# Kernel tuning notes

Hardware: AMD Instinct MI355X
Metric: run time of the kernel (lower is better)

Reference implementation:

```python
import jax, jax.numpy as jnp
import numpy as np

N_HEADS = 16
N_KV_HEADS = 4
HEAD_DIM = 128


def apply_rotary_emb(x, cos, sin):
    # x: [B, S, H, D]; cos/sin: [S, D//2]
    xr = x[..., 0::2]
    xi = x[..., 1::2]
    c = cos[None, :, None, :]
    s = sin[None, :, None, :]
    out_r = xr * c - xi * s
    out_i = xr * s + xi * c
    # interleave back: [..., D//2, 2] -> [..., D]
    return jnp.stack([out_r, out_i], axis=-1).reshape(x.shape)


def setup_inputs() -> dict:
    key = jax.random.key(0)
    ks = jax.random.split(key, 7)
    B, S, D = 4, 2048, 2048
    x = jax.random.normal(ks[0], (B, S, D), dtype=jnp.float32)
    # realistic rotary tables
    inv_freq = 1.0 / (10000.0 ** (jnp.arange(0, HEAD_DIM, 2, dtype=jnp.float32) / HEAD_DIM))
    t = jnp.arange(S, dtype=jnp.float32)
    freqs = jnp.outer(t, inv_freq)  # [S, D/2]
    freqs_cos = jnp.cos(freqs)
    freqs_sin = jnp.sin(freqs)
    sc = 0.02
    wq = jax.random.normal(ks[1], (D, N_HEADS * HEAD_DIM), dtype=jnp.float32) * sc
    wk = jax.random.normal(ks[2], (D, N_KV_HEADS * HEAD_DIM), dtype=jnp.float32) * sc
    wv = jax.random.normal(ks[3], (D, N_KV_HEADS * HEAD_DIM), dtype=jnp.float32) * sc
    wo = jax.random.normal(ks[4], (N_HEADS * HEAD_DIM, D), dtype=jnp.float32) * sc
    return {"x": x, "freqs_cos": freqs_cos, "freqs_sin": freqs_sin,
            "wq": wq, "wk": wk, "wv": wv, "wo": wo}


def reference(x, freqs_cos, freqs_sin, wq, wk, wv, wo):
    B, S, D = x.shape
    n_rep = N_HEADS // N_KV_HEADS
    xq = (x @ wq).reshape(B, S, N_HEADS, HEAD_DIM)
    xk = (x @ wk).reshape(B, S, N_KV_HEADS, HEAD_DIM)
    xv = (x @ wv).reshape(B, S, N_KV_HEADS, HEAD_DIM)
    xq = apply_rotary_emb(xq, freqs_cos, freqs_sin)
    xk = apply_rotary_emb(xk, freqs_cos, freqs_sin)
    # repeat_kv (GQA): [B,S,Hkv,D] -> [B,S,Hkv*n_rep,D]
    xk = jnp.repeat(xk, n_rep, axis=2)
    xv = jnp.repeat(xv, n_rep, axis=2)
    # [B,H,S,D]
    q = xq.transpose(0, 2, 1, 3)
    k = xk.transpose(0, 2, 1, 3)
    v = xv.transpose(0, 2, 1, 3)
    scores = jnp.einsum('bhqd,bhkd->bhqk', q, k) / jnp.sqrt(jnp.float32(HEAD_DIM))
    causal = jnp.triu(jnp.ones((S, S), dtype=bool), k=1)
    scores = jnp.where(causal[None, None], -jnp.inf, scores)
    probs = jax.nn.softmax(scores, axis=-1)
    out = jnp.einsum('bhqk,bhkd->bhqd', probs, v)
    out = out.transpose(0, 2, 1, 3).reshape(B, S, N_HEADS * HEAD_DIM)
    return out @ wo
```

## Files before the change

### kernel.cpp

```cpp
#include <hip/hip_runtime.h>
#include <stdint.h>
#include <stddef.h>

#define B_ 4
#define S_ 2048
#define D_ 2048
#define NH 16
#define NKV 4
#define HD 128
#define QKV_N 3072
#define ROWS (B_*S_)

typedef unsigned short u16;
typedef __attribute__((ext_vector_type(8))) unsigned short u16x8;
typedef __attribute__((ext_vector_type(8))) __bf16 bf16x8;
typedef __attribute__((ext_vector_type(4))) float f32x4;

__device__ __forceinline__ u16 f2bf(float f) {
  unsigned u = __builtin_bit_cast(unsigned, f);
  return (u16)((u + 0x7fffu + ((u >> 16) & 1u)) >> 16);
}
__device__ __forceinline__ float bf2f(u16 h) {
  return __builtin_bit_cast(float, (unsigned)h << 16);
}
__device__ __forceinline__ f32x4 mfma16(u16x8 a, u16x8 b, f32x4 c) {
  return __builtin_amdgcn_mfma_f32_16x16x32_bf16(
      __builtin_bit_cast(bf16x8, a), __builtin_bit_cast(bf16x8, b), c, 0, 0, 0);
}
__device__ __forceinline__ void gld16(const void* g, void* l) {
  __builtin_amdgcn_global_load_lds(
      (const __attribute__((address_space(1))) void*)g,
      (__attribute__((address_space(3))) void*)l, 16, 0, 0);
}

__global__ __launch_bounds__(256) void k_cast_x(const float* __restrict__ x, u16* __restrict__ xb) {
  int i = blockIdx.x * 256 + threadIdx.x;
  float4 v = ((const float4*)x)[i];
  union { u16 u[4]; uint2 p; } o;
  o.u[0] = f2bf(v.x); o.u[1] = f2bf(v.y); o.u[2] = f2bf(v.z); o.u[3] = f2bf(v.w);
  ((uint2*)xb)[i] = o.p;
}

__global__ __launch_bounds__(256) void k_wt(const float* __restrict__ w, u16* __restrict__ wt, int K, int N) {
  __shared__ float tile[32][33];
  int kb = blockIdx.y * 32, nb = blockIdx.x * 32;
  int tx = threadIdx.x, ty = threadIdx.y;
#pragma unroll
  for (int j = 0; j < 32; j += 8)
    tile[ty + j][tx] = w[(size_t)(kb + ty + j) * N + nb + tx];
  __syncthreads();
#pragma unroll
  for (int j = 0; j < 32; j += 8)
    wt[(size_t)(nb + ty + j) * K + kb + tx] = f2bf(tile[tx][ty + j]);
}


#define STG_A(KK, SS) do {                                                   \
    gld16(Ag + (size_t)r0 * 2048 + (KK) + coff, As + (SS) * 8192 + stl0);    \
    gld16(Ag + (size_t)(r0 + 128) * 2048 + (KK) + coff,                      \
          As + (SS) * 8192 + stl1);                                          \
  } while (0)
#define STG_B(KK, SS) do {                                                   \
    gld16(Bg + (size_t)r0 * 2048 + (KK) + coff, Bs + (SS) * 8192 + stl0);    \
    gld16(Bg + (size_t)(r0 + 128) * 2048 + (KK) + coff,                      \
          Bs + (SS) * 8192 + stl1);                                          \
  } while (0)

#define PHASE(RS, MB, RB, SS, SK, SA, VM) do {                               \
    const u16* Ap_ = As + (RS) * 8192;                                       \
    _Pragma("unroll") for (int i_ = 0; i_ < 4; ++i_)                         \
      af[i_] = *(const u16x8*)(Ap_ + arow0 + ((MB) + i_) * 512);             \
    if (RB) {                                                                \
      const u16* Bp_ = Bs + (RS) * 8192;                                     \
      _Pragma("unroll") for (int i_ = 0; i_ < 4; ++i_)                       \
        bf[i_] = *(const u16x8*)(Bp_ + brow0 + i_ * 512);                    \
    }                                                                        \
    if (SA) STG_A(SK, SS); else STG_B(SK, SS);                               \
    asm volatile("s_barrier" ::: "memory");                                  \
    asm volatile("s_waitcnt lgkmcnt(0)" ::: "memory");                       \
    __builtin_amdgcn_sched_barrier(0);                                       \
    __builtin_amdgcn_s_setprio(1);                                           \
    _Pragma("unroll") for (int i_ = 0; i_ < 4; ++i_)                         \
      _Pragma("unroll") for (int n_ = 0; n_ < 4; ++n_)                       \
        acc[(MB) + i_][n_] = mfma16(af[i_], bf[n_], acc[(MB) + i_][n_]);     \
    __builtin_amdgcn_s_setprio(0);                                           \
    __builtin_amdgcn_sched_barrier(0);                                       \
    if (VM) asm volatile("s_waitcnt vmcnt(8)" ::: "memory");                 \
    asm volatile("s_barrier" ::: "memory");                                  \
  } while (0)

template<int NT, bool F32OUT>
__global__ __launch_bounds__(512, 2) void k_gemm(const u16* __restrict__ A, const u16* __restrict__ Bt,
                                                 void* __restrict__ C) {
  __shared__ u16 As[4 * 8192];
  __shared__ u16 Bs[4 * 8192];
  int id = blockIdx.x;
  int nwg = gridDim.x;
  id = (id & 7) * (nwg >> 3) + (id >> 3);
  const int gx = NT / 256;
  int mb = (id / gx) * 256, nb = (id % gx) * 256;

  int t = threadIdx.x;
  int l = t & 63, L16 = l & 15, quad = l >> 4;
  int w = t >> 6, wm = w >> 2, wn = w & 3;
  const int schunk = 8 * (quad ^ ((L16 >> 1) & 3));
  const int arow0 = (wm * 128 + L16) * 32 + schunk;
  const int brow0 = (wn * 64 + L16) * 32 + schunk;
  const int r0 = t >> 2;
  const int coff = 8 * ((t & 3) ^ ((r0 >> 1) & 3));
  const int stl0 = (t & 448) * 8, stl1 = stl0 + 4096;

  const u16* Ag = A + (size_t)mb * 2048;
  const u16* Bg = Bt + (size_t)nb * 2048;
  u16x8 af[4], bf[4];
  f32x4 acc[8][4] = {};

  STG_A(0, 0);  STG_B(0, 0);
  STG_A(32, 1); STG_B(32, 1);
  STG_A(64, 2); STG_B(64, 2);
  asm volatile("s_waitcnt vmcnt(8)" ::: "memory");
  asm volatile("s_barrier" ::: "memory");

#pragma unroll 2
  for (int tt = 0; tt < 32; ++tt) {
    int rs0 = (2 * tt) & 3, rs1 = (2 * tt + 1) & 3;
    int ss1 = (2 * tt + 3) & 3;
    int k1n = ((tt + 1) & 31) * 64 + 32;
    int k0n = ((tt + 2) & 31) * 64;
    PHASE(rs0, 0, true,  ss1, k1n, true,  false);
    PHASE(rs0, 4, false, ss1, k1n, false, true);
    PHASE(rs1, 0, true,  rs0, k0n, true,  false);
    PHASE(rs1, 4, false, rs0, k0n, false, true);
  }
  asm volatile("s_waitcnt vmcnt(0)" ::: "memory");

#pragma unroll
  for (int m = 0; m < 8; ++m)
#pragma unroll
    for (int n = 0; n < 4; ++n)
#pragma unroll
      for (int r = 0; r < 4; ++r) {
        int row = mb + wm * 128 + m * 16 + quad * 4 + r;
        int col = nb + wn * 64 + n * 16 + L16;
        if constexpr (F32OUT)
          ((float*)C)[(size_t)row * NT + col] = acc[m][n][r];
        else
          ((u16*)C)[(size_t)row * NT + col] = f2bf(acc[m][n][r]);
      }
}

__global__ __launch_bounds__(256) void k_rope(const u16* __restrict__ qkv, const float* __restrict__ fc,
                                              const float* __restrict__ fs, u16* __restrict__ Q,
                                              u16* __restrict__ Kk) {
  const float SC = 0.1275174214f;
  int row = blockIdx.x;
  int b = row >> 11, s = row & 2047;
  int t = threadIdx.x;
#pragma unroll
  for (int j = 0; j < 5; ++j) {
    int p = t + j * 256;
    int i = p & 63;
    float c = fc[s * 64 + i], sn = fs[s * 64 + i];
    if (p < 1024) {
      int h = p >> 6;
      unsigned pr = *(const unsigned*)(qkv + (size_t)row * QKV_N + h * 128 + 2 * i);
      float xr = bf2f((u16)(pr & 0xffff)), xi = bf2f((u16)(pr >> 16));
      size_t o = (((size_t)(b * NH + h) * S_) + s) * HD + 2 * i;
      unsigned out = (unsigned)f2bf((xr * c - xi * sn) * SC) |
                     ((unsigned)f2bf((xr * sn + xi * c) * SC) << 16);
      *(unsigned*)(Q + o) = out;
    } else {
      int kh = (p - 1024) >> 6;
      unsigned pr = *(const unsigned*)(qkv + (size_t)row * QKV_N + 2048 + kh * 128 + 2 * i);
      float xr = bf2f((u16)(pr & 0xffff)), xi = bf2f((u16)(pr >> 16));
      size_t o = (((size_t)(b * NKV + kh) * S_) + s) * HD + 2 * i;
      unsigned out = (unsigned)f2bf(xr * c - xi * sn) | ((unsigned)f2bf(xr * sn + xi * c) << 16);
      *(unsigned*)(Kk + o) = out;
    }
  }
}

__global__ __launch_bounds__(256) void k_vt(const u16* __restrict__ qkv, u16* __restrict__ Vt) {
  __shared__ u16 tile[64 * 128];
  int blk = blockIdx.x;
  int sb = blk & 31, kh = (blk >> 5) & 3, b = blk >> 7;
  int t = threadIdx.x;
  int s0 = sb * 64;
#pragma unroll
  for (int i = 0; i < 4; ++i) {
    int lin = i * 256 + t;
    int row = lin >> 4, c = lin & 15;
    u16x8 v = *(const u16x8*)(qkv + (size_t)(b * S_ + s0 + row) * QKV_N + 2560 + kh * HD + c * 8);
    *(u16x8*)(tile + row * 128 + ((c ^ (row & 15)) * 8)) = v;
  }
  __syncthreads();
#pragma unroll
  for (int i = 0; i < 2; ++i) {
    int u = i * 256 + t;
    int p = u >> 3, o = u & 7;
    u16 lo[8], hi[8];
#pragma unroll
    for (int j = 0; j < 8; ++j) {
      int s = o * 8 + j;
      int cs = (p >> 2) ^ (s & 15);
      unsigned v = *(const unsigned*)(tile + s * 128 + cs * 8 + (p & 3) * 2);
      lo[j] = (u16)(v & 0xffff); hi[j] = (u16)(v >> 16);
    }
    size_t ob = ((size_t)(b * NKV + kh) * HD + 2 * p) * S_ + s0 + o * 8;
    *(u16x8*)(Vt + ob)      = *(u16x8*)lo;
    *(u16x8*)(Vt + ob + S_) = *(u16x8*)hi;
  }
}

__global__ __launch_bounds__(256) void k_attn(const u16* __restrict__ Q, const u16* __restrict__ Kg,
                                              const u16* __restrict__ Vt, u16* __restrict__ O) {
  int bx = blockIdx.x;
  int bh = bx >> 3, pr = bx & 7;
  int b = bh >> 4, h = bh & 15, kh = h >> 2;
  int t = threadIdx.x;
  int w = t >> 6, l = t & 63, L = l & 15, quad = l >> 4;

  __shared__ u16 Ks[64 * 128];
  __shared__ u16 Vs[128 * 64];
  __shared__ u16 Ps[4][32 * 72];
  u16* Pw = &Ps[w][0];

  const u16* Qh = Q  + ((size_t)(b * NH  + h ) * S_) * HD;
  const u16* Kh = Kg + ((size_t)(b * NKV + kh) * S_) * HD;
  const u16* Vh = Vt + ((size_t)(b * NKV + kh) * HD) * S_;

  u16x8 ones;
#pragma unroll
  for (int i = 0; i < 8; ++i) ones[i] = 0x3F80;

  int koff[4], voff[2];
#pragma unroll
  for (int kk = 0; kk < 4; ++kk) koff[kk] = 128 * L + 8 * ((4 * kk + quad) ^ (L & 7));
#pragma unroll
  for (int kc = 0; kc < 2; ++kc) voff[kc] = 64 * L + 8 * ((4 * kc + quad) ^ (L & 7));
  const int pread  = 72 * L + 8 * quad;
  const int pwrite = 72 * L + 4 * quad;

  int kgo[4], vgo[4], klo[4], vlo[4];
#pragma unroll
  for (int i = 0; i < 4; ++i) {
    int lin = i * 256 + t;
    int row = lin >> 4, c = lin & 15;
    kgo[i] = row * HD + ((c ^ (row & 7)) * 8);
    int d = lin >> 3, c2 = lin & 7;
    vgo[i] = d * S_ + ((c2 ^ (d & 7)) * 8);
    klo[i] = (i * 256 + (t & 192)) * 8;
    vlo[i] = (i * 256 + (t & 192)) * 8;
  }

#pragma unroll 1
  for (int half = 0; half < 2; ++half) {
    int qb = half ? (15 - pr) : pr;
    int q0 = qb * 128 + w * 32;

    u16x8 qf[2][4];
#pragma unroll
    for (int m = 0; m < 2; ++m)
#pragma unroll
      for (int kk = 0; kk < 4; ++kk)
        qf[m][kk] = *(const u16x8*)(Qh + (size_t)(q0 + m * 16 + L) * HD + kk * 32 + quad * 8);

    f32x4 acc[2][9] = {};
    int ktiles = 2 * qb + 2;
#pragma unroll 1
    for (int kt = 0; kt < ktiles; ++kt) {
      int kbase = kt * 64;
      __syncthreads();
      const u16* Kt = Kh + (size_t)kbase * HD;
      const u16* Vg = Vh + kbase;
#pragma unroll
      for (int i = 0; i < 4; ++i) gld16(Kt + kgo[i], Ks + klo[i]);
#pragma unroll
      for (int i = 0; i < 4; ++i) gld16(Vg + vgo[i], Vs + vlo[i]);
      __syncthreads();
      if (kbase > q0 + 31) continue;

      bool needMask = (kbase + 63 > q0);
#pragma unroll
      for (int n = 0; n < 4; ++n) {
        f32x4 s0v = {}, s1v = {};
#pragma unroll
        for (int kk = 0; kk < 4; ++kk) {
          u16x8 kf = *(const u16x8*)(Ks + koff[kk] + 2048 * n);
          s0v = mfma16(kf, qf[0][kk], s0v);
          s1v = mfma16(kf, qf[1][kk], s1v);
        }
#pragma unroll
        for (int m = 0; m < 2; ++m) {
          f32x4 sv = m ? s1v : s0v;
          int qrow = q0 + m * 16 + L;
          unsigned eu[4];
#pragma unroll
          for (int r = 0; r < 4; ++r) {
            float e = exp2f(sv[r]);
            if (needMask) {
              int key = kbase + n * 16 + quad * 4 + r;
              e = (key <= qrow) ? e : 0.0f;
            }
            eu[r] = __builtin_bit_cast(unsigned, e);
          }
          uint2 pk;
          pk.x = __builtin_amdgcn_perm(eu[1], eu[0], 0x07060302u);
          pk.y = __builtin_amdgcn_perm(eu[3], eu[2], 0x07060302u);
          *(uint2*)(Pw + pwrite + 1152 * m + 16 * n) = pk;
        }
      }
#pragma unroll
      for (int kc = 0; kc < 2; ++kc) {
        u16x8 pf0 = *(const u16x8*)(Pw + pread + 32 * kc);
        u16x8 pf1 = *(const u16x8*)(Pw + pread + 1152 + 32 * kc);
#pragma unroll
        for (int nt = 0; nt < 8; ++nt) {
          u16x8 vf = *(const u16x8*)(Vs + voff[kc] + 1024 * nt);
          acc[0][nt] = mfma16(pf0, vf, acc[0][nt]);
          acc[1][nt] = mfma16(pf1, vf, acc[1][nt]);
        }
        acc[0][8] = mfma16(pf0, ones, acc[0][8]);
        acc[1][8] = mfma16(pf1, ones, acc[1][8]);
      }
    }
#pragma unroll
    for (int m = 0; m < 2; ++m)
#pragma unroll
      for (int r = 0; r < 4; ++r) {
        float inv = 1.0f / acc[m][8][r];
        int qrow = q0 + m * 16 + quad * 4 + r;
#pragma unroll
        for (int nt = 0; nt < 8; ++nt) {
          int col = h * HD + nt * 16 + L;
          O[(size_t)(b * S_ + qrow) * D_ + col] = f2bf(acc[m][nt][r] * inv);
        }
      }
  }
}

extern "C" void kernel_launch(void* const* d_in, const int* in_sizes, int n_in,
                              void* d_out, int out_size, void* d_ws, size_t ws_size,
                              hipStream_t stream) {
  const float* x  = (const float*)d_in[0];
  const float* fc = (const float*)d_in[1];
  const float* fs = (const float*)d_in[2];
  const float* wq = (const float*)d_in[3];
  const float* wk = (const float*)d_in[4];
  const float* wv = (const float*)d_in[5];
  const float* wo = (const float*)d_in[6];
  float* out = (float*)d_out;

  u16* p = (u16*)d_ws;
  u16* xb    = p; p += (size_t)ROWS * D_;
  u16* wqkvT = p; p += (size_t)QKV_N * D_;
  u16* woT   = p; p += (size_t)D_ * D_;
  u16* qkv   = p; p += (size_t)ROWS * QKV_N;
  u16* Qr    = p; p += (size_t)ROWS * (NH * HD);
  u16* Kr    = p; p += (size_t)ROWS * (NKV * HD);
  u16* Vtr   = p; p += (size_t)ROWS * (NKV * HD);
  u16* AO    = p; p += (size_t)ROWS * D_;

  k_cast_x<<<dim3(ROWS * D_ / 1024), dim3(256), 0, stream>>>(x, xb);
  k_wt<<<dim3(64, 64), dim3(32, 8), 0, stream>>>(wq, wqkvT, 2048, 2048);
  k_wt<<<dim3(16, 64), dim3(32, 8), 0, stream>>>(wk, wqkvT + (size_t)2048 * 2048, 2048, 512);
  k_wt<<<dim3(16, 64), dim3(32, 8), 0, stream>>>(wv, wqkvT + (size_t)2560 * 2048, 2048, 512);
  k_wt<<<dim3(64, 64), dim3(32, 8), 0, stream>>>(wo, woT, 2048, 2048);
  k_gemm<QKV_N, false><<<dim3((QKV_N / 256) * (ROWS / 256)), dim3(512), 0, stream>>>(xb, wqkvT, qkv);
  k_rope<<<dim3(ROWS), dim3(256), 0, stream>>>(qkv, fc, fs, Qr, Kr);
  k_vt<<<dim3(B_ * NKV * (S_ / 64)), dim3(256), 0, stream>>>(qkv, Vtr);
  k_attn<<<dim3(64 * 8), dim3(256), 0, stream>>>(Qr, Kr, Vtr, AO);
  k_gemm<D_, true><<<dim3((D_ / 256) * (ROWS / 256)), dim3(512), 0, stream>>>(AO, woT, out);
}
```

Measured before the change: 458.8 us.

## Double-buffer LDS fragment registers to overlap LDS reads with MFMA in GEMM

```diff
diff --git a/kernel.cpp b/kernel.cpp
--- a/kernel.cpp
+++ b/kernel.cpp
@@ -66,26 +66,25 @@
           Bs + (SS) * 8192 + stl1);                                          \
   } while (0)
 
-#define PHASE(RS, MB, RB, SS, SK, SA, VM) do {                               \
-    const u16* Ap_ = As + (RS) * 8192;                                       \
+#define PH(AFU, BFU, MB, AFW, BFW, RDS, RDM, RDBF, SA, SK, SS, VM) do {      \
+    const u16* Rp_ = As + (RDS) * 8192;                                      \
     _Pragma("unroll") for (int i_ = 0; i_ < 4; ++i_)                         \
-      af[i_] = *(const u16x8*)(Ap_ + arow0 + ((MB) + i_) * 512);             \
-    if (RB) {                                                                \
-      const u16* Bp_ = Bs + (RS) * 8192;                                     \
+      AFW[i_] = *(const u16x8*)(Rp_ + arow0 + ((RDM) + i_) * 512);           \
+    if (RDBF) {                                                              \
+      const u16* Bp_ = Bs + (RDS) * 8192;                                    \
       _Pragma("unroll") for (int i_ = 0; i_ < 4; ++i_)                       \
-        bf[i_] = *(const u16x8*)(Bp_ + brow0 + i_ * 512);                    \
+        BFW[i_] = *(const u16x8*)(Bp_ + brow0 + i_ * 512);                   \
     }                                                                        \
     if (SA) STG_A(SK, SS); else STG_B(SK, SS);                               \
-    asm volatile("s_barrier" ::: "memory");                                  \
-    asm volatile("s_waitcnt lgkmcnt(0)" ::: "memory");                       \
     __builtin_amdgcn_sched_barrier(0);                                       \
     __builtin_amdgcn_s_setprio(1);                                           \
     _Pragma("unroll") for (int i_ = 0; i_ < 4; ++i_)                         \
       _Pragma("unroll") for (int n_ = 0; n_ < 4; ++n_)                       \
-        acc[(MB) + i_][n_] = mfma16(af[i_], bf[n_], acc[(MB) + i_][n_]);     \
+        acc[(MB) + i_][n_] = mfma16(AFU[i_], BFU[n_], acc[(MB) + i_][n_]);   \
     __builtin_amdgcn_s_setprio(0);                                           \
     __builtin_amdgcn_sched_barrier(0);                                       \
-    if (VM) asm volatile("s_waitcnt vmcnt(8)" ::: "memory");                 \
+    asm volatile("s_waitcnt lgkmcnt(0)" ::: "memory");                       \
+    if (VM) asm volatile("s_waitcnt vmcnt(6)" ::: "memory");                 \
     asm volatile("s_barrier" ::: "memory");                                  \
   } while (0)
 
@@ -112,7 +111,7 @@
 
   const u16* Ag = A + (size_t)mb * 2048;
   const u16* Bg = Bt + (size_t)nb * 2048;
-  u16x8 af[4], bf[4];
+  u16x8 afX[4], afY[4], bfX[4], bfY[4];
   f32x4 acc[8][4] = {};
 
   STG_A(0, 0);  STG_B(0, 0);
@@ -120,17 +119,25 @@
   STG_A(64, 2); STG_B(64, 2);
   asm volatile("s_waitcnt vmcnt(8)" ::: "memory");
   asm volatile("s_barrier" ::: "memory");
-
-#pragma unroll 2
-  for (int tt = 0; tt < 32; ++tt) {
-    int rs0 = (2 * tt) & 3, rs1 = (2 * tt + 1) & 3;
-    int ss1 = (2 * tt + 3) & 3;
-    int k1n = ((tt + 1) & 31) * 64 + 32;
-    int k0n = ((tt + 2) & 31) * 64;
-    PHASE(rs0, 0, true,  ss1, k1n, true,  false);
-    PHASE(rs0, 4, false, ss1, k1n, false, true);
-    PHASE(rs1, 0, true,  rs0, k0n, true,  false);
-    PHASE(rs1, 4, false, rs0, k0n, false, true);
+#pragma unroll
+  for (int i = 0; i < 4; ++i) {
+    afX[i] = *(const u16x8*)(As + arow0 + i * 512);
+    bfX[i] = *(const u16x8*)(Bs + brow0 + i * 512);
+  }
+
+#pragma unroll 1
+  for (int uu = 0; uu < 16; ++uu) {
+    int tA = 2 * uu, tB = 2 * uu + 1;
+    int a1 = ((tA + 1) & 31) * 64 + 32, a2 = ((tA + 2) & 31) * 64;
+    int b1 = ((tB + 1) & 31) * 64 + 32, b2 = ((tB + 2) & 31) * 64;
+    PH(afX, bfX, 0, afY, bfX, 0, 4, false, true,  a1, 3, true);
+    PH(afY, bfX, 4, afX, bfY, 1, 0, true,  false, a1, 3, false);
+    PH(afX, bfY, 0, afY, bfX, 1, 4, false, true,  a2, 0, true);
+    PH(afY, bfY, 4, afX, bfX, 2, 0, true,  false, a2, 0, false);
+    PH(afX, bfX, 0, afY, bfX, 2, 4, false, true,  b1, 1, true);
+    PH(afY, bfX, 4, afX, bfY, 3, 0, true,  false, b1, 1, false);
+    PH(afX, bfY, 0, afY, bfX, 3, 4, false, true,  b2, 2, true);
+    PH(afY, bfY, 4, afX, bfX, 0, 0, true,  false, b2, 2, false);
   }
   asm volatile("s_waitcnt vmcnt(0)" ::: "memory");
 
```

Measured after the change: 467.6 us. Within noise of the previous version (+1.9%).

## Restructure GEMM to 4 waves with 128x128 per-wave tiles

Applied to the files above, without the earlier changes.

```diff
diff --git a/kernel.cpp b/kernel.cpp
--- a/kernel.cpp
+++ b/kernel.cpp
@@ -55,42 +55,31 @@
 }
 
 
-#define STG_A(KK, SS) do {                                                   \
-    gld16(Ag + (size_t)r0 * 2048 + (KK) + coff, As + (SS) * 8192 + stl0);    \
-    gld16(Ag + (size_t)(r0 + 128) * 2048 + (KK) + coff,                      \
-          As + (SS) * 8192 + stl1);                                          \
+#define STG(GP, KK, SS, LB) do {                                             \
+    _Pragma("unroll") for (int j_ = 0; j_ < 4; ++j_)                         \
+      gld16(GP + (size_t)(j_ * 64 + r0) * 2048 + (KK) + coff,                \
+            LB + (SS) * 8192 + j_ * 2048 + stl);                             \
   } while (0)
-#define STG_B(KK, SS) do {                                                   \
-    gld16(Bg + (size_t)r0 * 2048 + (KK) + coff, Bs + (SS) * 8192 + stl0);    \
-    gld16(Bg + (size_t)(r0 + 128) * 2048 + (KK) + coff,                      \
-          Bs + (SS) * 8192 + stl1);                                          \
-  } while (0)
-
-#define PHASE(RS, MB, RB, SS, SK, SA, VM) do {                               \
+
+#define PH(RS, SS, KN) do {                                                  \
+    STG(Ag, KN, SS, As);                                                     \
+    STG(Bg, KN, SS, Bs);                                                     \
     const u16* Ap_ = As + (RS) * 8192;                                       \
-    _Pragma("unroll") for (int i_ = 0; i_ < 4; ++i_)                         \
-      af[i_] = *(const u16x8*)(Ap_ + arow0 + ((MB) + i_) * 512);             \
-    if (RB) {                                                                \
-      const u16* Bp_ = Bs + (RS) * 8192;                                     \
-      _Pragma("unroll") for (int i_ = 0; i_ < 4; ++i_)                       \
-        bf[i_] = *(const u16x8*)(Bp_ + brow0 + i_ * 512);                    \
-    }                                                                        \
-    if (SA) STG_A(SK, SS); else STG_B(SK, SS);                               \
-    asm volatile("s_barrier" ::: "memory");                                  \
-    asm volatile("s_waitcnt lgkmcnt(0)" ::: "memory");                       \
-    __builtin_amdgcn_sched_barrier(0);                                       \
-    __builtin_amdgcn_s_setprio(1);                                           \
-    _Pragma("unroll") for (int i_ = 0; i_ < 4; ++i_)                         \
-      _Pragma("unroll") for (int n_ = 0; n_ < 4; ++n_)                       \
-        acc[(MB) + i_][n_] = mfma16(af[i_], bf[n_], acc[(MB) + i_][n_]);     \
-    __builtin_amdgcn_s_setprio(0);                                           \
-    __builtin_amdgcn_sched_barrier(0);                                       \
-    if (VM) asm volatile("s_waitcnt vmcnt(8)" ::: "memory");                 \
+    const u16* Bp_ = Bs + (RS) * 8192;                                       \
+    u16x8 af_[8], bf_[8];                                                    \
+    _Pragma("unroll") for (int i_ = 0; i_ < 8; ++i_)                         \
+      af_[i_] = *(const u16x8*)(Ap_ + arow0 + i_ * 512);                     \
+    _Pragma("unroll") for (int i_ = 0; i_ < 8; ++i_)                         \
+      bf_[i_] = *(const u16x8*)(Bp_ + brow0 + i_ * 512);                     \
+    _Pragma("unroll") for (int m_ = 0; m_ < 8; ++m_)                         \
+      _Pragma("unroll") for (int n_ = 0; n_ < 8; ++n_)                       \
+        acc[m_][n_] = mfma16(af_[m_], bf_[n_], acc[m_][n_]);                 \
+    asm volatile("s_waitcnt vmcnt(8)" ::: "memory");                         \
     asm volatile("s_barrier" ::: "memory");                                  \
   } while (0)
 
 template<int NT, bool F32OUT>
-__global__ __launch_bounds__(512, 2) void k_gemm(const u16* __restrict__ A, const u16* __restrict__ Bt,
+__global__ __launch_bounds__(256, 1) void k_gemm(const u16* __restrict__ A, const u16* __restrict__ Bt,
                                                  void* __restrict__ C) {
   __shared__ u16 As[4 * 8192];
   __shared__ u16 Bs[4 * 8192];
@@ -102,46 +91,43 @@
 
   int t = threadIdx.x;
   int l = t & 63, L16 = l & 15, quad = l >> 4;
-  int w = t >> 6, wm = w >> 2, wn = w & 3;
+  int w = t >> 6, wm = w >> 1, wn = w & 1;
   const int schunk = 8 * (quad ^ ((L16 >> 1) & 3));
   const int arow0 = (wm * 128 + L16) * 32 + schunk;
-  const int brow0 = (wn * 64 + L16) * 32 + schunk;
+  const int brow0 = (wn * 128 + L16) * 32 + schunk;
   const int r0 = t >> 2;
   const int coff = 8 * ((t & 3) ^ ((r0 >> 1) & 3));
-  const int stl0 = (t & 448) * 8, stl1 = stl0 + 4096;
+  const int stl = (t & 192) * 8;
 
   const u16* Ag = A + (size_t)mb * 2048;
   const u16* Bg = Bt + (size_t)nb * 2048;
-  u16x8 af[4], bf[4];
-  f32x4 acc[8][4] = {};
-
-  STG_A(0, 0);  STG_B(0, 0);
-  STG_A(32, 1); STG_B(32, 1);
-  STG_A(64, 2); STG_B(64, 2);
+  f32x4 acc[8][8] = {};
+
+  STG(Ag, 0, 0, As);  STG(Bg, 0, 0, Bs);
+  STG(Ag, 32, 1, As); STG(Bg, 32, 1, Bs);
   asm volatile("s_waitcnt vmcnt(8)" ::: "memory");
   asm volatile("s_barrier" ::: "memory");
 
-#pragma unroll 2
-  for (int tt = 0; tt < 32; ++tt) {
-    int rs0 = (2 * tt) & 3, rs1 = (2 * tt + 1) & 3;
-    int ss1 = (2 * tt + 3) & 3;
-    int k1n = ((tt + 1) & 31) * 64 + 32;
-    int k0n = ((tt + 2) & 31) * 64;
-    PHASE(rs0, 0, true,  ss1, k1n, true,  false);
-    PHASE(rs0, 4, false, ss1, k1n, false, true);
-    PHASE(rs1, 0, true,  rs0, k0n, true,  false);
-    PHASE(rs1, 4, false, rs0, k0n, false, true);
+#pragma unroll 1
+  for (int tp = 0; tp < 16; ++tp) {
+    int e = 2 * tp, o = 2 * tp + 1;
+    int ke = ((e + 1) & 31) * 64;
+    int ko = ((o + 1) & 31) * 64;
+    PH(0, 2, ke);
+    PH(1, 3, ke + 32);
+    PH(2, 0, ko);
+    PH(3, 1, ko + 32);
   }
   asm volatile("s_waitcnt vmcnt(0)" ::: "memory");
 
 #pragma unroll
   for (int m = 0; m < 8; ++m)
 #pragma unroll
-    for (int n = 0; n < 4; ++n)
+    for (int n = 0; n < 8; ++n)
 #pragma unroll
       for (int r = 0; r < 4; ++r) {
         int row = mb + wm * 128 + m * 16 + quad * 4 + r;
-        int col = nb + wn * 64 + n * 16 + L16;
+        int col = nb + wn * 128 + n * 16 + L16;
         if constexpr (F32OUT)
           ((float*)C)[(size_t)row * NT + col] = acc[m][n][r];
         else
@@ -366,9 +352,9 @@
   k_wt<<<dim3(16, 64), dim3(32, 8), 0, stream>>>(wk, wqkvT + (size_t)2048 * 2048, 2048, 512);
   k_wt<<<dim3(16, 64), dim3(32, 8), 0, stream>>>(wv, wqkvT + (size_t)2560 * 2048, 2048, 512);
   k_wt<<<dim3(64, 64), dim3(32, 8), 0, stream>>>(wo, woT, 2048, 2048);
-  k_gemm<QKV_N, false><<<dim3((QKV_N / 256) * (ROWS / 256)), dim3(512), 0, stream>>>(xb, wqkvT, qkv);
+  k_gemm<QKV_N, false><<<dim3((QKV_N / 256) * (ROWS / 256)), dim3(256), 0, stream>>>(xb, wqkvT, qkv);
   k_rope<<<dim3(ROWS), dim3(256), 0, stream>>>(qkv, fc, fs, Qr, Kr);
   k_vt<<<dim3(B_ * NKV * (S_ / 64)), dim3(256), 0, stream>>>(qkv, Vtr);
   k_attn<<<dim3(64 * 8), dim3(256), 0, stream>>>(Qr, Kr, Vtr, AO);
-  k_gemm<D_, true><<<dim3((D_ / 256) * (ROWS / 256)), dim3(512), 0, stream>>>(AO, woT, out);
-}
+  k_gemm<D_, true><<<dim3((D_ / 256) * (ROWS / 256)), dim3(256), 0, stream>>>(AO, woT, out);
+}
```

New measurement: 517.6 us. 1.13x slower.
